# Performance work log

Measured on AMD Instinct MI355X. Metric: run time of the kernel, lower is better.

The kernel has to match this reference:

```python
import jax, jax.numpy as jnp
import numpy as np

N = 50000        # num_nodes
D = 512          # input_dim == output_dim (residual update requires equality)
EU = 100000      # undirected edges; directed E = 2*EU = 200000
STEP = 0.5       # step_size


def setup_inputs() -> dict:
    key = jax.random.key(0)
    ks = jax.random.split(key, 5)
    x = jax.random.normal(ks[0], (N, D), jnp.float32)
    # symmetric edge list without self loops: store (s,d) then (d,s)
    src = jax.random.randint(ks[1], (EU,), 0, N, dtype=jnp.int32)
    off = jax.random.randint(ks[2], (EU,), 1, N, dtype=jnp.int32)
    dst = (src + off) % N
    edge_index = jnp.stack([jnp.concatenate([src, dst]),
                            jnp.concatenate([dst, src])])  # [2, 2*EU]
    # reverse-edge index: edge e < EU reverses to e+EU and vice versa
    ar = jnp.arange(EU, dtype=jnp.int32)
    right_idx = jnp.concatenate([ar + EU, ar])
    # params: nn.Linear(D, D) and sheaf_learner nn.Linear(2D, 1, bias=False)
    W_lin = jax.random.normal(ks[3], (D, D), jnp.float32) / np.sqrt(D)
    b_lin = jnp.zeros((D,), jnp.float32)
    w_sheaf = jax.random.normal(ks[4], (2 * D,), jnp.float32) / np.sqrt(2 * D)
    return {"x": x, "W_lin": W_lin, "b_lin": b_lin, "w_sheaf": w_sheaf,
            "edge_index": edge_index, "right_idx": right_idx}


def reference(x, W_lin, b_lin, w_sheaf, edge_index, right_idx):
    row, col = edge_index[0], edge_index[1]
    d = x.shape[1]
    # sheaf_learner(cat([x_row, x_col])) == (x @ w[:d])[row] + (x @ w[d:])[col]
    s = x @ w_sheaf[:d]                      # [N]
    t = x @ w_sheaf[d:]                      # [N]
    maps = jnp.tanh(s[row] + t[col])         # [E] scalar restriction maps
    # off-diagonal Laplacian values: -F_e(row) * F_reverse(e)
    non_diag = -maps * maps[right_idx]       # [E]
    diag_maps = jax.ops.segment_sum(maps ** 2, row, num_segments=N)  # [N]
    d_inv = (diag_maps + 1.0) ** -0.5        # [N]
    norm_maps = d_inv[row] * non_diag * d_inv[col]                   # [E]
    diag = d_inv * diag_maps * d_inv                                 # [N]
    # y = linear(x); L @ y done as diag term + edge scatter
    y = x @ W_lin.T + b_lin                  # [N, D]
    Ly = diag[:, None] * y + jax.ops.segment_sum(
        norm_maps[:, None] * y[col], row, num_segments=N)
    return x - STEP * Ly
```

## Files before the change

### kernel.cpp

```cpp
#include <hip/hip_runtime.h>
#include <hip/hip_bf16.h>
#include <cstdint>
#include <cstddef>


#define DD 512
#define STEPSZ 0.5f
#define SLOTS 32

typedef __bf16 bf16;
typedef __bf16 bf16x8 __attribute__((ext_vector_type(8)));
typedef __bf16 bf16x4 __attribute__((ext_vector_type(4)));
typedef float f32x4 __attribute__((ext_vector_type(4)));

#define GLOAD16(g, l)                                                     \
  __builtin_amdgcn_global_load_lds(                                       \
      (const __attribute__((address_space(1))) void*)(g),                 \
      (__attribute__((address_space(3))) void*)(l), 16, 0, 0)

__global__ __launch_bounds__(256) void k_convert_w(
    const float* __restrict__ w, bf16* __restrict__ wbf, int n) {
  int i = (blockIdx.x * 256 + threadIdx.x) * 4;
  if (i >= n) return;
  float4 v = *(const float4*)(w + i);
  bf16x4 p;
  p[0] = (bf16)v.x; p[1] = (bf16)v.y; p[2] = (bf16)v.z; p[3] = (bf16)v.w;
  *(bf16x4*)(wbf + i) = p;
}

__global__ __launch_bounds__(256) void k_convert_st(
    const float* __restrict__ x, const float* __restrict__ wsheaf,
    bf16* __restrict__ xbf, float* __restrict__ s, float* __restrict__ t,
    int n) {
  int lane = threadIdx.x & 63;
  int row = (blockIdx.x << 2) + (threadIdx.x >> 6);
  if (row >= n) return;
  const float* xr = x + (size_t)row * DD + lane * 8;
  float4 a = *(const float4*)xr;
  float4 b = *(const float4*)(xr + 4);
  bf16x8 p;
  p[0] = (bf16)a.x; p[1] = (bf16)a.y; p[2] = (bf16)a.z; p[3] = (bf16)a.w;
  p[4] = (bf16)b.x; p[5] = (bf16)b.y; p[6] = (bf16)b.z; p[7] = (bf16)b.w;
  *(bf16x8*)(xbf + (size_t)row * DD + lane * 8) = p;
  const float* w1 = wsheaf + lane * 8;
  const float* w2 = wsheaf + DD + lane * 8;
  float4 wa = *(const float4*)w1, wb = *(const float4*)(w1 + 4);
  float4 wc = *(const float4*)w2, wd = *(const float4*)(w2 + 4);
  float sv = a.x * wa.x + a.y * wa.y + a.z * wa.z + a.w * wa.w +
             b.x * wb.x + b.y * wb.y + b.z * wb.z + b.w * wb.w;
  float tv = a.x * wc.x + a.y * wc.y + a.z * wc.z + a.w * wc.w +
             b.x * wd.x + b.y * wd.y + b.z * wd.z + b.w * wd.w;
  #pragma unroll
  for (int o = 32; o > 0; o >>= 1) {
    sv += __shfl_xor(sv, o);
    tv += __shfl_xor(tv, o);
  }
  if (lane == 0) { s[row] = sv; t[row] = tv; }
}

__global__ __launch_bounds__(256) void k_edge_maps(
    const int* __restrict__ ei, const float* __restrict__ s,
    const float* __restrict__ t, float* __restrict__ diag_maps, int E) {
  int e = blockIdx.x * 256 + threadIdx.x;
  if (e >= E) return;
  int r = ei[e], c = ei[E + e];
  float m = tanhf(s[r] + t[c]);
  atomicAdd(diag_maps + r, m * m);
}

__global__ __launch_bounds__(256) void k_csr_fill(
    const int* __restrict__ ei, const float* __restrict__ s,
    const float* __restrict__ t, const float* __restrict__ dmaps,
    int* __restrict__ fill, int* __restrict__ ccol, float* __restrict__ cval,
    int E) {
  int e = blockIdx.x * 256 + threadIdx.x;
  if (e >= E) return;
  int r = ei[e], c = ei[E + e];
  float me = tanhf(s[r] + t[c]);
  float mr = tanhf(s[c] + t[r]);
  float nm = -me * mr * rsqrtf((dmaps[r] + 1.0f) * (dmaps[c] + 1.0f));
  int p = atomicAdd(fill + r, 1);
  if (p < SLOTS) {
    ccol[(size_t)r * SLOTS + p] = c;
    cval[(size_t)r * SLOTS + p] = nm;
  }
}

__global__ __launch_bounds__(256) void k_gemm(
    const bf16* __restrict__ xbf, const bf16* __restrict__ wbf,
    const float* __restrict__ bias, bf16* __restrict__ y, int M, int nwg) {
  __shared__ bf16 lds[16384];
  int orig = blockIdx.x;
  int q = nwg >> 3, r = nwg & 7;
  int xcd = orig & 7;
  int wgid = (xcd < r ? xcd * (q + 1) : r * (q + 1) + (xcd - r) * q) +
             (orig >> 3);
  int bm = wgid >> 2, bn = wgid & 3;
  int tid = threadIdx.x, w = tid >> 6, lane = tid & 63;
  int wr = w >> 1, wc = w & 1;
  int l7 = lane & 7, lhi = lane >> 4;

  int srow = lane >> 3;
  int kc = l7 ^ srow;
  const bf16* gA[4];
  const bf16* gB[4];
  bf16* lA[4];
  bf16* lB[4];
  #pragma unroll
  for (int j = 0; j < 4; ++j) {
    int rloc = w * 32 + j * 8 + srow;
    int ga = bm * 128 + rloc;
    if (ga > M - 1) ga = M - 1;
    gA[j] = xbf + (size_t)ga * DD + kc * 8;
    gB[j] = wbf + (size_t)(bn * 128 + rloc) * DD + kc * 8;
    lA[j] = lds + (w * 32 + j * 8) * 64;
    lB[j] = lds + 8192 + (w * 32 + j * 8) * 64;
  }

  f32x4 acc[4][4] = {};
  int arow = (wr * 64 + (lane & 15)) * 64;
  int brow = (wc * 64 + (lane & 15)) * 64;

  for (int k0 = 0; k0 < DD; k0 += 64) {
    #pragma unroll
    for (int j = 0; j < 4; ++j) {
      GLOAD16(gA[j] + k0, lA[j]);
      GLOAD16(gB[j] + k0, lB[j]);
    }
    __syncthreads();
    #pragma unroll
    for (int kw = 0; kw < 2; ++kw) {
      int sl = ((kw * 4 + lhi) ^ l7) * 8;
      bf16x8 af[4], bfr[4];
      #pragma unroll
      for (int m = 0; m < 4; ++m)
        af[m] = *(const bf16x8*)(lds + arow + m * 16 * 64 + sl);
      #pragma unroll
      for (int nn = 0; nn < 4; ++nn)
        bfr[nn] = *(const bf16x8*)(lds + 8192 + brow + nn * 16 * 64 + sl);
      #pragma unroll
      for (int m = 0; m < 4; ++m)
        #pragma unroll
        for (int nn = 0; nn < 4; ++nn)
          acc[m][nn] = __builtin_amdgcn_mfma_f32_16x16x32_bf16(
              af[m], bfr[nn], acc[m][nn], 0, 0, 0);
    }
    __syncthreads();
  }

  float bv[4];
  #pragma unroll
  for (int nn = 0; nn < 4; ++nn)
    bv[nn] = bias[bn * 128 + wc * 64 + nn * 16 + (lane & 15)];
  bf16* reg = lds + w * 4096;
  #pragma unroll
  for (int m = 0; m < 4; ++m)
    #pragma unroll
    for (int nn = 0; nn < 4; ++nn)
      #pragma unroll
      for (int rr = 0; rr < 4; ++rr) {
        int row = m * 16 + lhi * 4 + rr;
        int col = nn * 16 + (lane & 15);
        reg[row * 64 + (((col >> 3) ^ (row & 7)) << 3) + (col & 7)] =
            (bf16)(acc[m][nn][rr] + bv[nn]);
      }
  #pragma unroll
  for (int p = 0; p < 8; ++p) {
    int row = p * 8 + (lane >> 3);
    int slot = l7 ^ (row & 7);
    bf16x8 v = *(const bf16x8*)(reg + row * 64 + slot * 8);
    int grow = bm * 128 + wr * 64 + row;
    if (grow < M)
      *(bf16x8*)(y + (size_t)grow * DD + bn * 128 + wc * 64 + l7 * 8) = v;
  }
}

__global__ __launch_bounds__(256) void k_final(
    const float* __restrict__ x, const bf16* __restrict__ y,
    const float* __restrict__ dmaps, const int* __restrict__ fill,
    const int* __restrict__ ccol, const float* __restrict__ cval,
    float* __restrict__ out, int n) {
  int lane = threadIdx.x & 63;
  int row = (blockIdx.x << 2) + (threadIdx.x >> 6);
  if (row >= n) return;
  int c0 = lane * 8;
  bf16x8 yv = *(const bf16x8*)(y + (size_t)row * DD + c0);
  float dm = dmaps[row];
  float dg = dm / (dm + 1.0f);
  float acc[8];
  #pragma unroll
  for (int j = 0; j < 8; ++j) acc[j] = dg * (float)yv[j];
  int cnt = fill[row];
  if (cnt > SLOTS) cnt = SLOTS;
  const int* cc = ccol + (size_t)row * SLOTS;
  const float* cv = cval + (size_t)row * SLOTS;
  for (int i = 0; i < cnt; ++i) {
    int c = cc[i];
    float v = cv[i];
    bf16x8 nv = *(const bf16x8*)(y + (size_t)c * DD + c0);
    #pragma unroll
    for (int j = 0; j < 8; ++j) acc[j] += v * (float)nv[j];
  }
  const float* xr = x + (size_t)row * DD + c0;
  float4 xa = *(const float4*)xr, xb = *(const float4*)(xr + 4);
  float4 o1, o2;
  o1.x = xa.x - STEPSZ * acc[0]; o1.y = xa.y - STEPSZ * acc[1];
  o1.z = xa.z - STEPSZ * acc[2]; o1.w = xa.w - STEPSZ * acc[3];
  o2.x = xb.x - STEPSZ * acc[4]; o2.y = xb.y - STEPSZ * acc[5];
  o2.z = xb.z - STEPSZ * acc[6]; o2.w = xb.w - STEPSZ * acc[7];
  float* outr = out + (size_t)row * DD + c0;
  *(float4*)outr = o1;
  *(float4*)(outr + 4) = o2;
}

extern "C" void kernel_launch(void* const* d_in, const int* in_sizes, int n_in,
                              void* d_out, int out_size, void* d_ws,
                              size_t ws_size, hipStream_t stream) {
  const float* x = (const float*)d_in[0];
  const float* W = (const float*)d_in[1];
  const float* b = (const float*)d_in[2];
  const float* wsheaf = (const float*)d_in[3];
  const int* ei = (const int*)d_in[4];
  const int* right = (const int*)d_in[5];
  (void)right;
  int N = in_sizes[0] / DD;
  int E = in_sizes[5];

  char* ws = (char*)d_ws;
  size_t p = 0;
  auto alloc = [&](size_t bytes) -> char* {
    char* r = ws + p;
    p += (bytes + 255) & ~(size_t)255;
    return r;
  };
  bf16* yb = (bf16*)alloc((size_t)N * DD * 2);
  float* cval = (float*)alloc((size_t)N * SLOTS * 4);
  int* ccol = (int*)alloc((size_t)N * SLOTS * 4);
  float* s = (float*)alloc((size_t)N * 4);
  float* t = (float*)alloc((size_t)N * 4);
  bf16* wbf = (bf16*)alloc((size_t)DD * DD * 2);
  char* zblock = alloc((size_t)N * 8);
  float* diag_maps = (float*)zblock;
  int* fill = (int*)(zblock + (size_t)N * 4);

  bf16* xbf = (bf16*)d_out;

  hipMemsetAsync(zblock, 0, (size_t)N * 8, stream);
  k_convert_w<<<(DD * DD / 4 + 255) / 256, 256, 0, stream>>>(W, wbf, DD * DD);
  k_convert_st<<<(N + 3) / 4, 256, 0, stream>>>(x, wsheaf, xbf, s, t, N);
  k_edge_maps<<<(E + 255) / 256, 256, 0, stream>>>(ei, s, t, diag_maps, E);
  k_csr_fill<<<(E + 255) / 256, 256, 0, stream>>>(ei, s, t, diag_maps, fill,
                                                  ccol, cval, E);
  int MT = (N + 127) / 128;
  int nwg = MT * 4;
  k_gemm<<<nwg, 256, 0, stream>>>(xbf, wbf, b, yb, N, nwg);
  k_final<<<(N + 3) / 4, 256, 0, stream>>>(x, yb, diag_maps, fill, ccol, cval,
                                           (float*)d_out, N);
}
```

Baseline: 179.8 us.

## Fuse edge passes by deferring normalization and gather residual from bf16 x

The two per-edge kernels become one. It accumulates diag_maps with atomics and stores only the unnormalized -m_e*m_rev value in the CSR slots. The d_inv[row]*d_inv[col] normalization moves into the final gather kernel. That gather now reads column indices and values four at a time and issues four neighbor row loads per iteration. When workspace allows, the bf16 copy of x gets its own buffer, and the final kernel reads the residual x from it instead of the fp32 input. This halves that read but adds bf16 rounding error to the output.

```diff
diff --git a/kernel.cpp b/kernel.cpp
--- a/kernel.cpp
+++ b/kernel.cpp
@@ -58,31 +58,22 @@
   if (lane == 0) { s[row] = sv; t[row] = tv; }
 }
 
-__global__ __launch_bounds__(256) void k_edge_maps(
+__global__ __launch_bounds__(256) void k_fill(
     const int* __restrict__ ei, const float* __restrict__ s,
-    const float* __restrict__ t, float* __restrict__ diag_maps, int E) {
-  int e = blockIdx.x * 256 + threadIdx.x;
-  if (e >= E) return;
-  int r = ei[e], c = ei[E + e];
-  float m = tanhf(s[r] + t[c]);
-  atomicAdd(diag_maps + r, m * m);
-}
-
-__global__ __launch_bounds__(256) void k_csr_fill(
-    const int* __restrict__ ei, const float* __restrict__ s,
-    const float* __restrict__ t, const float* __restrict__ dmaps,
+    const float* __restrict__ t, float* __restrict__ dmaps,
     int* __restrict__ fill, int* __restrict__ ccol, float* __restrict__ cval,
     int E) {
   int e = blockIdx.x * 256 + threadIdx.x;
   if (e >= E) return;
   int r = ei[e], c = ei[E + e];
-  float me = tanhf(s[r] + t[c]);
-  float mr = tanhf(s[c] + t[r]);
-  float nm = -me * mr * rsqrtf((dmaps[r] + 1.0f) * (dmaps[c] + 1.0f));
+  float sr = s[r], tc = t[c], sc = s[c], tr = t[r];
+  float me = tanhf(sr + tc);
+  float mr = tanhf(sc + tr);
+  atomicAdd(dmaps + r, me * me);
   int p = atomicAdd(fill + r, 1);
   if (p < SLOTS) {
     ccol[(size_t)r * SLOTS + p] = c;
-    cval[(size_t)r * SLOTS + p] = nm;
+    cval[(size_t)r * SLOTS + p] = -me * mr;
   }
 }
 
@@ -176,16 +167,18 @@
 }
 
 __global__ __launch_bounds__(256) void k_final(
-    const float* __restrict__ x, const bf16* __restrict__ y,
-    const float* __restrict__ dmaps, const int* __restrict__ fill,
-    const int* __restrict__ ccol, const float* __restrict__ cval,
-    float* __restrict__ out, int n) {
+    const float* __restrict__ x, const bf16* __restrict__ xb,
+    const bf16* __restrict__ y, const float* __restrict__ dmaps,
+    const int* __restrict__ fill, const int* __restrict__ ccol,
+    const float* __restrict__ cval, float* __restrict__ out, int n,
+    int use_bf) {
   int lane = threadIdx.x & 63;
   int row = (blockIdx.x << 2) + (threadIdx.x >> 6);
   if (row >= n) return;
   int c0 = lane * 8;
   bf16x8 yv = *(const bf16x8*)(y + (size_t)row * DD + c0);
   float dm = dmaps[row];
+  float inv_r = rsqrtf(dm + 1.0f);
   float dg = dm / (dm + 1.0f);
   float acc[8];
   #pragma unroll
@@ -194,20 +187,44 @@
   if (cnt > SLOTS) cnt = SLOTS;
   const int* cc = ccol + (size_t)row * SLOTS;
   const float* cv = cval + (size_t)row * SLOTS;
-  for (int i = 0; i < cnt; ++i) {
-    int c = cc[i];
-    float v = cv[i];
-    bf16x8 nv = *(const bf16x8*)(y + (size_t)c * DD + c0);
-    #pragma unroll
-    for (int j = 0; j < 8; ++j) acc[j] += v * (float)nv[j];
-  }
-  const float* xr = x + (size_t)row * DD + c0;
-  float4 xa = *(const float4*)xr, xb = *(const float4*)(xr + 4);
+  unsigned nm1 = (unsigned)(n - 1);
+  for (int i = 0; i < cnt; i += 4) {
+    int4 c4 = *(const int4*)(cc + i);
+    float4 v4 = *(const float4*)(cv + i);
+    int rem = cnt - i;
+    unsigned ca = min((unsigned)c4.x, nm1);
+    unsigned cb = min((unsigned)c4.y, nm1);
+    unsigned cg = min((unsigned)c4.z, nm1);
+    unsigned cd = min((unsigned)c4.w, nm1);
+    bf16x8 na = *(const bf16x8*)(y + (size_t)ca * DD + c0);
+    bf16x8 nb = *(const bf16x8*)(y + (size_t)cb * DD + c0);
+    bf16x8 ng = *(const bf16x8*)(y + (size_t)cg * DD + c0);
+    bf16x8 nd = *(const bf16x8*)(y + (size_t)cd * DD + c0);
+    float va = rem > 0 ? v4.x * inv_r * rsqrtf(dmaps[ca] + 1.0f) : 0.0f;
+    float vb = rem > 1 ? v4.y * inv_r * rsqrtf(dmaps[cb] + 1.0f) : 0.0f;
+    float vg = rem > 2 ? v4.z * inv_r * rsqrtf(dmaps[cg] + 1.0f) : 0.0f;
+    float vd = rem > 3 ? v4.w * inv_r * rsqrtf(dmaps[cd] + 1.0f) : 0.0f;
+    #pragma unroll
+    for (int j = 0; j < 8; ++j)
+      acc[j] += va * (float)na[j] + vb * (float)nb[j] + vg * (float)ng[j] +
+                vd * (float)nd[j];
+  }
+  float xr[8];
+  if (use_bf) {
+    bf16x8 xv = *(const bf16x8*)(xb + (size_t)row * DD + c0);
+    #pragma unroll
+    for (int j = 0; j < 8; ++j) xr[j] = (float)xv[j];
+  } else {
+    const float* xp = x + (size_t)row * DD + c0;
+    float4 xa = *(const float4*)xp, xbv = *(const float4*)(xp + 4);
+    xr[0] = xa.x; xr[1] = xa.y; xr[2] = xa.z; xr[3] = xa.w;
+    xr[4] = xbv.x; xr[5] = xbv.y; xr[6] = xbv.z; xr[7] = xbv.w;
+  }
   float4 o1, o2;
-  o1.x = xa.x - STEPSZ * acc[0]; o1.y = xa.y - STEPSZ * acc[1];
-  o1.z = xa.z - STEPSZ * acc[2]; o1.w = xa.w - STEPSZ * acc[3];
-  o2.x = xb.x - STEPSZ * acc[4]; o2.y = xb.y - STEPSZ * acc[5];
-  o2.z = xb.z - STEPSZ * acc[6]; o2.w = xb.w - STEPSZ * acc[7];
+  o1.x = xr[0] - STEPSZ * acc[0]; o1.y = xr[1] - STEPSZ * acc[1];
+  o1.z = xr[2] - STEPSZ * acc[2]; o1.w = xr[3] - STEPSZ * acc[3];
+  o2.x = xr[4] - STEPSZ * acc[4]; o2.y = xr[5] - STEPSZ * acc[5];
+  o2.z = xr[6] - STEPSZ * acc[6]; o2.w = xr[7] - STEPSZ * acc[7];
   float* outr = out + (size_t)row * DD + c0;
   *(float4*)outr = o1;
   *(float4*)(outr + 4) = o2;
@@ -243,17 +260,18 @@
   float* diag_maps = (float*)zblock;
   int* fill = (int*)(zblock + (size_t)N * 4);
 
-  bf16* xbf = (bf16*)d_out;
+  size_t xbf_bytes = (size_t)N * DD * 2;
+  int use_bf = (p + xbf_bytes) <= ws_size;
+  bf16* xbf = use_bf ? (bf16*)alloc(xbf_bytes) : (bf16*)d_out;
 
   hipMemsetAsync(zblock, 0, (size_t)N * 8, stream);
   k_convert_w<<<(DD * DD / 4 + 255) / 256, 256, 0, stream>>>(W, wbf, DD * DD);
   k_convert_st<<<(N + 3) / 4, 256, 0, stream>>>(x, wsheaf, xbf, s, t, N);
-  k_edge_maps<<<(E + 255) / 256, 256, 0, stream>>>(ei, s, t, diag_maps, E);
-  k_csr_fill<<<(E + 255) / 256, 256, 0, stream>>>(ei, s, t, diag_maps, fill,
-                                                  ccol, cval, E);
+  k_fill<<<(E + 255) / 256, 256, 0, stream>>>(ei, s, t, diag_maps, fill, ccol,
+                                              cval, E);
   int MT = (N + 127) / 128;
   int nwg = MT * 4;
   k_gemm<<<nwg, 256, 0, stream>>>(xbf, wbf, b, yb, N, nwg);
-  k_final<<<(N + 3) / 4, 256, 0, stream>>>(x, yb, diag_maps, fill, ccol, cval,
-                                           (float*)d_out, N);
-}
+  k_final<<<(N + 3) / 4, 256, 0, stream>>>(x, xbf, yb, diag_maps, fill, ccol,
+                                           cval, (float*)d_out, N, use_bf);
+}
```

After: 168.9 us. 1.06x faster.
